# Kernel optimization log

Measured on AMD Instinct MI355X. Metric: run time of the kernel, lower is better.

## Reference

```python
import jax, jax.numpy as jnp
import numpy as np

D_MODEL = 2048
N_Q = 16
N_KV = 4
HEAD_DIM = 128
WINDOW = 512
ROPE_BASE = 10000.0


def _rope_cos_sin(T, dtype):
    half = HEAD_DIM // 2
    inv_freq = 1.0 / (ROPE_BASE ** (jnp.arange(0, half, dtype=jnp.float32) * 2.0 / HEAD_DIM))
    pos = jnp.arange(T, dtype=jnp.float32)
    ang = pos[:, None] * inv_freq[None, :]            # [T, half]
    emb = jnp.concatenate([ang, ang], axis=-1)        # [T, HEAD_DIM]
    return jnp.cos(emb).astype(dtype), jnp.sin(emb).astype(dtype)


def _rotate_half(x):
    x1, x2 = jnp.split(x, 2, axis=-1)
    return jnp.concatenate([-x2, x1], axis=-1)


def _apply_rope(t, cos, sin):
    # t: [B, H, T, hd]; cos/sin: [T, hd]
    return t * cos[None, None, :, :] + _rotate_half(t) * sin[None, None, :, :]


def setup_inputs() -> dict:
    key = jax.random.key(0)
    ks = jax.random.split(key, 5)
    s = 0.02
    return {
        "x": jax.random.normal(ks[0], (2, 2048, D_MODEL), dtype=jnp.float32),
        "wq": jax.random.normal(ks[1], (D_MODEL, N_Q * HEAD_DIM), dtype=jnp.float32) * s,
        "wk": jax.random.normal(ks[2], (D_MODEL, N_KV * HEAD_DIM), dtype=jnp.float32) * s,
        "wv": jax.random.normal(ks[3], (D_MODEL, N_KV * HEAD_DIM), dtype=jnp.float32) * s,
        "wo": jax.random.normal(ks[4], (N_Q * HEAD_DIM, D_MODEL), dtype=jnp.float32) * s,
    }


def reference(x, wq, wk, wv, wo):
    B, T, _ = x.shape
    q = (x @ wq).reshape(B, T, N_Q, HEAD_DIM).transpose(0, 2, 1, 3)    # [B,Hq,T,hd]
    k = (x @ wk).reshape(B, T, N_KV, HEAD_DIM).transpose(0, 2, 1, 3)   # [B,Hkv,T,hd]
    v = (x @ wv).reshape(B, T, N_KV, HEAD_DIM).transpose(0, 2, 1, 3)

    cos, sin = _rope_cos_sin(T, x.dtype)
    q = _apply_rope(q, cos, sin)
    k = _apply_rope(k, cos, sin)

    # GQA: repeat_interleave kv heads to match q heads
    g = N_Q // N_KV
    k = jnp.repeat(k, g, axis=1)
    v = jnp.repeat(v, g, axis=1)

    scale = 1.0 / np.sqrt(HEAD_DIM)
    scores = jnp.einsum("bhqd,bhkd->bhqk", q, k) * scale

    idx = jnp.arange(T)
    diff = idx[:, None] - idx[None, :]
    keep = (diff >= 0) & (diff < WINDOW)               # causal & sliding window
    scores = jnp.where(keep[None, None, :, :], scores, jnp.finfo(scores.dtype).min)
    attn = jax.nn.softmax(scores, axis=-1)

    out = jnp.einsum("bhqk,bhkd->bhqd", attn, v)       # [B,Hq,T,hd]
    out = out.transpose(0, 2, 1, 3).reshape(B, T, N_Q * HEAD_DIM)
    return out @ wo
```

## Files before the change

### kernel.cpp

```cpp
#include <hip/hip_runtime.h>

#define T_SEQ   2048
#define DM      2048
#define N_Q     16
#define N_KV    4
#define HD      128
#define WIN     512
#define NB      2
#define NQKV    3072
#define QK_SCALE_L2E 0.12751744f

typedef short bf16x8 __attribute__((ext_vector_type(8)));
typedef float f32x4  __attribute__((ext_vector_type(4)));
typedef float f32x16 __attribute__((ext_vector_type(16)));
typedef unsigned short us4v __attribute__((ext_vector_type(4)));

__device__ __forceinline__ unsigned short f2bf(float f) {
    union { float f; unsigned u; } v; v.f = f;
    unsigned u = v.u;
    u += 0x7fffu + ((u >> 16) & 1u);
    return (unsigned short)(u >> 16);
}
__device__ __forceinline__ float bf2f(unsigned short h) {
    union { unsigned u; float f; } v; v.u = ((unsigned)h) << 16;
    return v.f;
}
__device__ __forceinline__ unsigned cvt_pk_bf16(float a, float b) {
    unsigned r;
    asm("v_cvt_pk_bf16_f32 %0, %1, %2" : "=v"(r) : "v"(a), "v"(b));
    return r;
}

#define GLOAD_LDS16(g, l) __builtin_amdgcn_global_load_lds( \
    (const __attribute__((address_space(1))) void*)(g),     \
    (__attribute__((address_space(3))) void*)(l), 16, 0, 0)

struct us4 { unsigned short a, b, c, d; };


__global__ __launch_bounds__(256)
void prep_a(const float* __restrict__ x, const float* __restrict__ wq,
            const float* __restrict__ wk, const float* __restrict__ wv,
            const float* __restrict__ wo,
            unsigned short* __restrict__ xbf, unsigned short* __restrict__ wqkvT,
            unsigned short* __restrict__ woT,
            float* __restrict__ cosT, float* __restrict__ sinT) {
    __shared__ float tile[32][33];
    int blk = blockIdx.x;
    if (blk < 8192) {
        long i = ((long)blk * 256 + threadIdx.x) * 4;
        float4 f = *(const float4*)(x + i);
        us4 o; o.a = f2bf(f.x); o.b = f2bf(f.y); o.c = f2bf(f.z); o.d = f2bf(f.w);
        *(us4*)(xbf + i) = o;
        return;
    }
    blk -= 8192;
    if (blk < 10240) {
        const float* in; unsigned short* outp; int C, bx, by;
        if (blk < 4096)      { in = wq; outp = wqkvT;                         C = DM;  bx = blk & 63;          by = blk >> 6; }
        else if (blk < 5120) { int k = blk - 4096; in = wk; outp = wqkvT + (long)DM * DM;         C = 512; bx = k & 15; by = k >> 4; }
        else if (blk < 6144) { int k = blk - 5120; in = wv; outp = wqkvT + (long)(DM + 512) * DM; C = 512; bx = k & 15; by = k >> 4; }
        else                 { int k = blk - 6144; in = wo; outp = woT;                           C = DM;  bx = k & 63; by = k >> 6; }
        const int c0 = bx * 32, r0 = by * 32;
        const int tx = threadIdx.x & 31, ty = threadIdx.x >> 5;
#pragma unroll
        for (int i = 0; i < 4; ++i)
            tile[ty + i * 8][tx] = in[(long)(r0 + ty + i * 8) * C + c0 + tx];
        __syncthreads();
#pragma unroll
        for (int i = 0; i < 4; ++i)
            outp[(long)(c0 + ty + i * 8) * DM + r0 + tx] = f2bf(tile[tx][ty + i * 8]);
        return;
    }
    blk -= 10240;
    const int idx = blk * 256 + threadIdx.x;
    const int t = idx >> 6, d = idx & 63;
    const float inv = __expf(-(float)d * (9.210340371976184f / 64.0f));
    const float ang = (float)t * inv;
    cosT[idx] = cosf(ang);
    sinT[idx] = sinf(ang);
}


__global__ __launch_bounds__(256)
void prep_b(unsigned short* __restrict__ qkv,
            const float* __restrict__ cosT, const float* __restrict__ sinT,
            unsigned short* __restrict__ vt) {
    __shared__ unsigned short stile[32][33];
    int blk = blockIdx.x;
    if (blk < 5120) {
        const int idx = blk * 256 + threadIdx.x;
        const int d4 = (idx & 15) * 4;
        const int hh = (idx >> 4) % 20;
        const int row = idx / (16 * 20);
        const int t = row & (T_SEQ - 1);
        const int col = (hh < N_Q) ? hh * HD + d4 : DM + (hh - N_Q) * HD + d4;
        unsigned short* p = qkv + (long)row * NQKV + col;
        us4v a = *(const us4v*)p;
        us4v b = *(const us4v*)(p + 64);
        float4 c = *(const float4*)&cosT[t * 64 + d4];
        float4 s = *(const float4*)&sinT[t * 64 + d4];
        const float sc = (hh < N_Q) ? QK_SCALE_L2E : 1.0f;
        us4v o1, o2;
        const float cc[4] = { c.x, c.y, c.z, c.w }, ss[4] = { s.x, s.y, s.z, s.w };
#pragma unroll
        for (int i = 0; i < 4; ++i) {
            const float av = bf2f(a[i]), bv = bf2f(b[i]);
            o1[i] = f2bf((av * cc[i] - bv * ss[i]) * sc);
            o2[i] = f2bf((bv * cc[i] + av * ss[i]) * sc);
        }
        *(us4v*)p        = o1;
        *(us4v*)(p + 64) = o2;
        return;
    }
    blk -= 5120;
    const int bh = blk >> 8;
    const int d0 = ((blk >> 6) & 3) * 32;
    const int t0 = (blk & 63) * 32;
    const int tx = threadIdx.x & 31, ty = threadIdx.x >> 5;
    const long inbase = (long)(bh >> 2) * T_SEQ;
    const int coff = DM + N_KV * HD + (bh & 3) * HD;
#pragma unroll
    for (int i = 0; i < 4; ++i)
        stile[ty + i * 8][tx] = qkv[(inbase + t0 + ty + i * 8) * NQKV + coff + d0 + tx];
    __syncthreads();
#pragma unroll
    for (int i = 0; i < 4; ++i)
        vt[((long)bh * HD + d0 + ty + i * 8) * T_SEQ + t0 + tx] = stile[tx][ty + i * 8];
}


template<int OUT_BF16>
__global__ __launch_bounds__(256)
void gemm_bt(const unsigned short* __restrict__ A,
             const unsigned short* __restrict__ Bt,
             void* __restrict__ Cvoid, int K, int ldc) {
    __shared__ __align__(16) unsigned short sA[128 * 64];
    __shared__ __align__(16) unsigned short sB[128 * 64];
    const int tid = threadIdx.x;
    const int lane = tid & 63;
    const int wid = tid >> 6;
    const int wr = (wid >> 1) * 64, wc = (wid & 1) * 64;
    const int l5 = lane >> 5, l31 = lane & 31;

    const int gx = gridDim.x;
    const int nwg = gx * gridDim.y;
    int flat = blockIdx.y * gx + blockIdx.x;
    flat = (flat & 7) * (nwg >> 3) + (flat >> 3);
    const long Arow0 = (long)(flat / gx) * 128;
    const long Brow0 = (long)(flat % gx) * 128;

    f32x16 acc[2][2] = {};

    for (int kt = 0; kt < K; kt += 64) {
        __syncthreads();
#pragma unroll
        for (int n = 0; n < 4; ++n) {
            const int linb = n * 256 + wid * 64;
            const int lin  = linb + lane;
            const int row  = lin >> 3;
            const int sw   = (row ^ (row >> 3)) & 7;
            const int sc   = (lin & 7) ^ sw;
            const unsigned short* gA = A  + (Arow0 + row) * K + kt + sc * 8;
            const unsigned short* gB = Bt + (Brow0 + row) * K + kt + sc * 8;
            GLOAD_LDS16(gA, &sA[linb * 8]);
            GLOAD_LDS16(gB, &sB[linb * 8]);
        }
        __syncthreads();
#pragma unroll
        for (int kc = 0; kc < 4; ++kc) {
            bf16x8 av[2], bv[2];
#pragma unroll
            for (int t = 0; t < 2; ++t) {
                const int rowa = wr + t * 32 + l31;
                const int ca = (kc * 2 + l5) ^ ((rowa ^ (rowa >> 3)) & 7);
                av[t] = *(const bf16x8*)&sA[rowa * 64 + ca * 8];
                const int rowb = wc + t * 32 + l31;
                const int cb = (kc * 2 + l5) ^ ((rowb ^ (rowb >> 3)) & 7);
                bv[t] = *(const bf16x8*)&sB[rowb * 64 + cb * 8];
            }
#pragma unroll
            for (int ti = 0; ti < 2; ++ti)
#pragma unroll
                for (int tj = 0; tj < 2; ++tj)
                    acc[ti][tj] = __builtin_amdgcn_mfma_f32_32x32x16_bf16(av[ti], bv[tj], acc[ti][tj], 0, 0, 0);
        }
    }

#pragma unroll
    for (int ti = 0; ti < 2; ++ti)
#pragma unroll
        for (int tj = 0; tj < 2; ++tj)
#pragma unroll
            for (int r = 0; r < 16; ++r) {
                const long row = Arow0 + wr + ti * 32 + (r & 3) + 8 * (r >> 2) + 4 * l5;
                const long col = Brow0 + wc + tj * 32 + l31;
                if (OUT_BF16)
                    ((unsigned short*)Cvoid)[row * ldc + col] = f2bf(acc[ti][tj][r]);
                else
                    ((float*)Cvoid)[row * ldc + col] = acc[ti][tj][r];
            }
}


__global__ __launch_bounds__(512, 2)
void attn_kernel(const unsigned short* __restrict__ qkv,
                 const unsigned short* __restrict__ vt,
                 unsigned short* __restrict__ aout) {
    const int qt = blockIdx.x, hkv = blockIdx.y, b = blockIdx.z;
    const int tid = threadIdx.x, lane = tid & 63, w = tid >> 6;
    const int qh = hkv * 4 + (w & 3);
    const int qsub = w >> 2;
    const int q0w = qt * 64 + qsub * 32;
    const int lo = lane & 15, hi = lane >> 4;

    __shared__ __align__(16) unsigned short sK[2][64 * 128];
    __shared__ __align__(16) unsigned short sV[2][128 * 64];
    __shared__ __align__(16) unsigned short plds[8][32 * 64];
    unsigned short* pl = plds[w];

    bf16x8 qf2[2][4];
#pragma unroll
    for (int f = 0; f < 2; ++f) {
        const unsigned short* qp = qkv + (long)(b * T_SEQ + q0w + f * 16 + lo) * NQKV + qh * HD + hi * 8;
#pragma unroll
        for (int s = 0; s < 4; ++s) qf2[f][s] = *(const bf16x8*)(qp + s * 32);
    }

    f32x4 of[8][2] = {};
    float m_r[2] = { -1e30f, -1e30f };
    float s_r[2] = { 0.f, 0.f };

    int kstart = qt * 64 - (WIN - 1);
    if (kstart < 0) kstart = 0;
    kstart &= ~63;
    const int kend = qt * 64 + 63;

    const unsigned short* kbase = qkv + (long)b * T_SEQ * NQKV + DM + hkv * HD;
    const unsigned short* vbase = vt + (long)(b * N_KV + hkv) * HD * T_SEQ;

    int kr[2], kc[2], vr[2], vc[2];
#pragma unroll
    for (int u = 0; u < 2; ++u) {
        const int c = u * 512 + tid;
        kr[u] = c >> 4;  kc[u] = (c & 15) ^ (kr[u] & 7);
        vr[u] = c >> 3;  vc[u] = (c & 7) ^ (vr[u] & 7);
    }

#define STAGE(bf, kt_) do {                                                              \
    _Pragma("unroll")                                                                    \
    for (int u = 0; u < 2; ++u) {                                                        \
        const int dbase = (u * 512 + w * 64) * 8;                                        \
        GLOAD_LDS16(kbase + (long)((kt_) + kr[u]) * NQKV + kc[u] * 8, &sK[bf][dbase]);   \
        GLOAD_LDS16(vbase + (long)vr[u] * T_SEQ + (kt_) + vc[u] * 8, &sV[bf][dbase]);    \
    } } while (0)

    STAGE(0, kstart);
    asm volatile("s_waitcnt vmcnt(0)" ::: "memory");
    __syncthreads();

    int buf = 0;
    for (int kt = kstart; kt <= kend; kt += 64) {
        if (kt + 64 <= kend) STAGE(buf ^ 1, kt + 64);

        f32x4 sf[4][2] = {};
        __builtin_amdgcn_s_setprio(1);
#pragma unroll
        for (int n = 0; n < 4; ++n) {
            const int row = n * 16 + lo;
#pragma unroll
            for (int s = 0; s < 4; ++s) {
                const int c = (s * 4 + hi) ^ (row & 7);
                bf16x8 kf = *(const bf16x8*)&sK[buf][row * 128 + c * 8];
                sf[n][0] = __builtin_amdgcn_mfma_f32_16x16x32_bf16(kf, qf2[0][s], sf[n][0], 0, 0, 0);
                sf[n][1] = __builtin_amdgcn_mfma_f32_16x16x32_bf16(kf, qf2[1][s], sf[n][1], 0, 0, 0);
            }
        }
        __builtin_amdgcn_s_setprio(0);

        const bool nomask = ((kt + 63) <= q0w) && ((q0w + 31 - kt) < WIN);

        float pv[2][4][4];
        float mx[2] = { -1e30f, -1e30f };
        if (nomask) {
#pragma unroll
            for (int f = 0; f < 2; ++f)
#pragma unroll
                for (int n = 0; n < 4; ++n)
#pragma unroll
                    for (int r = 0; r < 4; ++r) {
                        pv[f][n][r] = sf[n][f][r];
                        mx[f] = fmaxf(mx[f], pv[f][n][r]);
                    }
        } else {
#pragma unroll
            for (int f = 0; f < 2; ++f) {
                const int q = q0w + f * 16 + lo;
#pragma unroll
                for (int n = 0; n < 4; ++n)
#pragma unroll
                    for (int r = 0; r < 4; ++r) {
                        const int d = q - (kt + n * 16 + hi * 4 + r);
                        pv[f][n][r] = (d >= 0 && d < WIN) ? sf[n][f][r] : -1e30f;
                        mx[f] = fmaxf(mx[f], pv[f][n][r]);
                    }
            }
        }
#pragma unroll
        for (int f = 0; f < 2; ++f) {
            mx[f] = fmaxf(mx[f], __shfl_xor(mx[f], 16));
            mx[f] = fmaxf(mx[f], __shfl_xor(mx[f], 32));
        }

        const bool ok = (mx[0] <= m_r[0] + 8.0f) && (mx[1] <= m_r[1] + 8.0f);
        if (!__all(ok)) {
#pragma unroll
            for (int f = 0; f < 2; ++f) {
                const float mnew = fmaxf(m_r[f], mx[f]);
                const float resc = exp2f(m_r[f] - mnew);
                s_r[f] *= resc;
                m_r[f] = mnew;
                float r4[4];
#pragma unroll
                for (int r = 0; r < 4; ++r) r4[r] = __shfl(resc, hi * 4 + r);
#pragma unroll
                for (int j = 0; j < 8; ++j) {
                    of[j][f][0] *= r4[0]; of[j][f][1] *= r4[1];
                    of[j][f][2] *= r4[2]; of[j][f][3] *= r4[3];
                }
            }
        }

#pragma unroll
        for (int f = 0; f < 2; ++f) {
            float psum = 0.f;
#pragma unroll
            for (int n = 0; n < 4; ++n)
#pragma unroll
                for (int r = 0; r < 4; ++r) {
                    pv[f][n][r] = exp2f(pv[f][n][r] - m_r[f]);
                    psum += pv[f][n][r];
                }
            psum += __shfl_xor(psum, 16);
            psum += __shfl_xor(psum, 32);
            s_r[f] += psum;
        }

        const int swz = (lo & 7) << 3;
#pragma unroll
        for (int f = 0; f < 2; ++f) {
            const int rowq = f * 16 + lo;
#pragma unroll
            for (int n = 0; n < 4; ++n) {
                const int k0 = n * 16 + hi * 4;
                *(unsigned*)&pl[rowq * 64 + (k0 ^ swz)]       = cvt_pk_bf16(pv[f][n][0], pv[f][n][1]);
                *(unsigned*)&pl[rowq * 64 + ((k0 + 2) ^ swz)] = cvt_pk_bf16(pv[f][n][2], pv[f][n][3]);
            }
        }
        asm volatile("s_waitcnt lgkmcnt(0)" ::: "memory");
        __builtin_amdgcn_sched_barrier(0);
        bf16x8 pa2[2][2];
#pragma unroll
        for (int f = 0; f < 2; ++f)
#pragma unroll
            for (int ks = 0; ks < 2; ++ks) {
                const int c = (ks * 4 + hi) ^ (lo & 7);
                pa2[f][ks] = *(const bf16x8*)&pl[(f * 16 + lo) * 64 + c * 8];
            }

        __builtin_amdgcn_s_setprio(1);
#pragma unroll
        for (int j = 0; j < 8; ++j) {
            const int row = j * 16 + lo;
#pragma unroll
            for (int ks = 0; ks < 2; ++ks) {
                const int c = (ks * 4 + hi) ^ (row & 7);
                bf16x8 vf = *(const bf16x8*)&sV[buf][row * 64 + c * 8];
                of[j][0] = __builtin_amdgcn_mfma_f32_16x16x32_bf16(pa2[0][ks], vf, of[j][0], 0, 0, 0);
                of[j][1] = __builtin_amdgcn_mfma_f32_16x16x32_bf16(pa2[1][ks], vf, of[j][1], 0, 0, 0);
            }
        }
        __builtin_amdgcn_s_setprio(0);

        asm volatile("s_waitcnt vmcnt(0)" ::: "memory");
        __syncthreads();
        buf ^= 1;
    }
#undef STAGE

#pragma unroll
    for (int f = 0; f < 2; ++f) {
        float s4[4];
#pragma unroll
        for (int r = 0; r < 4; ++r) s4[r] = __shfl(s_r[f], hi * 4 + r);
#pragma unroll
        for (int r = 0; r < 4; ++r) {
            const int qrow = q0w + f * 16 + hi * 4 + r;
            const float inv = 1.0f / s4[r];
            unsigned short* op = aout + (long)(b * T_SEQ + qrow) * DM + qh * HD + lo;
#pragma unroll
            for (int j = 0; j < 8; ++j) op[j * 16] = f2bf(of[j][f][r] * inv);
        }
    }
}


extern "C" void kernel_launch(void* const* d_in, const int* in_sizes, int n_in,
                              void* d_out, int out_size, void* d_ws, size_t ws_size,
                              hipStream_t stream) {
    (void)in_sizes; (void)n_in; (void)out_size; (void)ws_size;
    const float* x  = (const float*)d_in[0];
    const float* wq = (const float*)d_in[1];
    const float* wk = (const float*)d_in[2];
    const float* wv = (const float*)d_in[3];
    const float* wo = (const float*)d_in[4];
    float* out = (float*)d_out;
    char* ws = (char*)d_ws;

    unsigned short* xbf   = (unsigned short*)(ws);
    unsigned short* wqkvT = (unsigned short*)(ws + 16777216);
    unsigned short* woT   = (unsigned short*)(ws + 29360128);
    unsigned short* qkv   = (unsigned short*)(ws + 37748736);
    unsigned short* vt    = (unsigned short*)(ws + 62914560);
    unsigned short* aout  = (unsigned short*)(ws + 67108864);
    float* cosT = (float*)(ws + 83886080);
    float* sinT = (float*)(ws + 84410368);

    prep_a<<<dim3(18944), dim3(256), 0, stream>>>(x, wq, wk, wv, wo, xbf, wqkvT, woT, cosT, sinT);
    gemm_bt<1><<<dim3(NQKV / 128, 32), dim3(256), 0, stream>>>(xbf, wqkvT, qkv, DM, NQKV);
    prep_b<<<dim3(7168), dim3(256), 0, stream>>>(qkv, cosT, sinT, vt);
    attn_kernel<<<dim3(T_SEQ / 64, 4, 2), dim3(512), 0, stream>>>(qkv, vt, aout);
    gemm_bt<0><<<dim3(DM / 128, 32), dim3(256), 0, stream>>>(aout, woT, out, DM, DM);
}
```

Baseline: 162.8 us.

## Fuse RoPE and Q scaling into the QKV GEMM epilogue

The QKV projection GEMM becomes a specialized kernel whose warps own columns d and d+64 of each head, so the RoPE rotation and the Q scale are applied to the fp32 accumulators before the bf16 store. The prep_b kernel shrinks to only the V transpose. This removes a full read-modify-write pass over Q and K and one double bf16 rounding, in exchange for strided B-operand fragment reads and cos/sin loads in the GEMM epilogue.

```diff
diff --git a/kernel.cpp b/kernel.cpp
--- a/kernel.cpp
+++ b/kernel.cpp
@@ -83,37 +83,9 @@
 
 
 __global__ __launch_bounds__(256)
-void prep_b(unsigned short* __restrict__ qkv,
-            const float* __restrict__ cosT, const float* __restrict__ sinT,
-            unsigned short* __restrict__ vt) {
+void prep_b(const unsigned short* __restrict__ qkv, unsigned short* __restrict__ vt) {
     __shared__ unsigned short stile[32][33];
-    int blk = blockIdx.x;
-    if (blk < 5120) {
-        const int idx = blk * 256 + threadIdx.x;
-        const int d4 = (idx & 15) * 4;
-        const int hh = (idx >> 4) % 20;
-        const int row = idx / (16 * 20);
-        const int t = row & (T_SEQ - 1);
-        const int col = (hh < N_Q) ? hh * HD + d4 : DM + (hh - N_Q) * HD + d4;
-        unsigned short* p = qkv + (long)row * NQKV + col;
-        us4v a = *(const us4v*)p;
-        us4v b = *(const us4v*)(p + 64);
-        float4 c = *(const float4*)&cosT[t * 64 + d4];
-        float4 s = *(const float4*)&sinT[t * 64 + d4];
-        const float sc = (hh < N_Q) ? QK_SCALE_L2E : 1.0f;
-        us4v o1, o2;
-        const float cc[4] = { c.x, c.y, c.z, c.w }, ss[4] = { s.x, s.y, s.z, s.w };
-#pragma unroll
-        for (int i = 0; i < 4; ++i) {
-            const float av = bf2f(a[i]), bv = bf2f(b[i]);
-            o1[i] = f2bf((av * cc[i] - bv * ss[i]) * sc);
-            o2[i] = f2bf((bv * cc[i] + av * ss[i]) * sc);
-        }
-        *(us4v*)p        = o1;
-        *(us4v*)(p + 64) = o2;
-        return;
-    }
-    blk -= 5120;
+    const int blk = blockIdx.x;
     const int bh = blk >> 8;
     const int d0 = ((blk >> 6) & 3) * 32;
     const int t0 = (blk & 63) * 32;
@@ -130,17 +102,19 @@
 }
 
 
-template<int OUT_BF16>
 __global__ __launch_bounds__(256)
-void gemm_bt(const unsigned short* __restrict__ A,
-             const unsigned short* __restrict__ Bt,
-             void* __restrict__ Cvoid, int K, int ldc) {
+void gemm_qkv(const unsigned short* __restrict__ A,
+              const unsigned short* __restrict__ Bt,
+              unsigned short* __restrict__ C,
+              const float* __restrict__ cosT, const float* __restrict__ sinT) {
+    const int K = DM, ldc = NQKV;
     __shared__ __align__(16) unsigned short sA[128 * 64];
     __shared__ __align__(16) unsigned short sB[128 * 64];
     const int tid = threadIdx.x;
     const int lane = tid & 63;
     const int wid = tid >> 6;
-    const int wr = (wid >> 1) * 64, wc = (wid & 1) * 64;
+    const int wr  = (wid >> 1) * 64;
+    const int wcs = (wid & 1) * 32;
     const int l5 = lane >> 5, l31 = lane & 31;
 
     const int gx = gridDim.x;
@@ -175,6 +149,94 @@
                 const int rowa = wr + t * 32 + l31;
                 const int ca = (kc * 2 + l5) ^ ((rowa ^ (rowa >> 3)) & 7);
                 av[t] = *(const bf16x8*)&sA[rowa * 64 + ca * 8];
+                const int rowb = wcs + t * 64 + l31;
+                const int cb = (kc * 2 + l5) ^ ((rowb ^ (rowb >> 3)) & 7);
+                bv[t] = *(const bf16x8*)&sB[rowb * 64 + cb * 8];
+            }
+#pragma unroll
+            for (int ti = 0; ti < 2; ++ti)
+#pragma unroll
+                for (int tj = 0; tj < 2; ++tj)
+                    acc[ti][tj] = __builtin_amdgcn_mfma_f32_32x32x16_bf16(av[ti], bv[tj], acc[ti][tj], 0, 0, 0);
+        }
+    }
+
+    const int hb = (int)(Brow0 >> 7);
+    if (hb < 20) {
+        const float sc = (hb < 16) ? QK_SCALE_L2E : 1.0f;
+        const int d6 = wcs + l31;
+        const long colL = Brow0 + d6;
+#pragma unroll
+        for (int ti = 0; ti < 2; ++ti)
+#pragma unroll
+            for (int r = 0; r < 16; ++r) {
+                const long row = Arow0 + wr + ti * 32 + (r & 3) + 8 * (r >> 2) + 4 * l5;
+                const int t = (int)(row & (T_SEQ - 1));
+                const float c = cosT[t * 64 + d6];
+                const float s = sinT[t * 64 + d6];
+                const float a = acc[ti][0][r], b = acc[ti][1][r];
+                C[row * ldc + colL]      = f2bf((a * c - b * s) * sc);
+                C[row * ldc + colL + 64] = f2bf((b * c + a * s) * sc);
+            }
+    } else {
+#pragma unroll
+        for (int ti = 0; ti < 2; ++ti)
+#pragma unroll
+            for (int tj = 0; tj < 2; ++tj)
+#pragma unroll
+                for (int r = 0; r < 16; ++r) {
+                    const long row = Arow0 + wr + ti * 32 + (r & 3) + 8 * (r >> 2) + 4 * l5;
+                    const long col = Brow0 + wcs + tj * 64 + l31;
+                    C[row * ldc + col] = f2bf(acc[ti][tj][r]);
+                }
+    }
+}
+
+
+__global__ __launch_bounds__(256)
+void gemm_bt(const unsigned short* __restrict__ A,
+             const unsigned short* __restrict__ Bt,
+             float* __restrict__ C, int K, int ldc) {
+    __shared__ __align__(16) unsigned short sA[128 * 64];
+    __shared__ __align__(16) unsigned short sB[128 * 64];
+    const int tid = threadIdx.x;
+    const int lane = tid & 63;
+    const int wid = tid >> 6;
+    const int wr = (wid >> 1) * 64, wc = (wid & 1) * 64;
+    const int l5 = lane >> 5, l31 = lane & 31;
+
+    const int gx = gridDim.x;
+    const int nwg = gx * gridDim.y;
+    int flat = blockIdx.y * gx + blockIdx.x;
+    flat = (flat & 7) * (nwg >> 3) + (flat >> 3);
+    const long Arow0 = (long)(flat / gx) * 128;
+    const long Brow0 = (long)(flat % gx) * 128;
+
+    f32x16 acc[2][2] = {};
+
+    for (int kt = 0; kt < K; kt += 64) {
+        __syncthreads();
+#pragma unroll
+        for (int n = 0; n < 4; ++n) {
+            const int linb = n * 256 + wid * 64;
+            const int lin  = linb + lane;
+            const int row  = lin >> 3;
+            const int sw   = (row ^ (row >> 3)) & 7;
+            const int sc   = (lin & 7) ^ sw;
+            const unsigned short* gA = A  + (Arow0 + row) * K + kt + sc * 8;
+            const unsigned short* gB = Bt + (Brow0 + row) * K + kt + sc * 8;
+            GLOAD_LDS16(gA, &sA[linb * 8]);
+            GLOAD_LDS16(gB, &sB[linb * 8]);
+        }
+        __syncthreads();
+#pragma unroll
+        for (int kc = 0; kc < 4; ++kc) {
+            bf16x8 av[2], bv[2];
+#pragma unroll
+            for (int t = 0; t < 2; ++t) {
+                const int rowa = wr + t * 32 + l31;
+                const int ca = (kc * 2 + l5) ^ ((rowa ^ (rowa >> 3)) & 7);
+                av[t] = *(const bf16x8*)&sA[rowa * 64 + ca * 8];
                 const int rowb = wc + t * 32 + l31;
                 const int cb = (kc * 2 + l5) ^ ((rowb ^ (rowb >> 3)) & 7);
                 bv[t] = *(const bf16x8*)&sB[rowb * 64 + cb * 8];
@@ -195,10 +257,7 @@
             for (int r = 0; r < 16; ++r) {
                 const long row = Arow0 + wr + ti * 32 + (r & 3) + 8 * (r >> 2) + 4 * l5;
                 const long col = Brow0 + wc + tj * 32 + l31;
-                if (OUT_BF16)
-                    ((unsigned short*)Cvoid)[row * ldc + col] = f2bf(acc[ti][tj][r]);
-                else
-                    ((float*)Cvoid)[row * ldc + col] = acc[ti][tj][r];
+                C[row * ldc + col] = acc[ti][tj][r];
             }
 }
 
@@ -427,8 +486,8 @@
     float* sinT = (float*)(ws + 84410368);
 
     prep_a<<<dim3(18944), dim3(256), 0, stream>>>(x, wq, wk, wv, wo, xbf, wqkvT, woT, cosT, sinT);
-    gemm_bt<1><<<dim3(NQKV / 128, 32), dim3(256), 0, stream>>>(xbf, wqkvT, qkv, DM, NQKV);
-    prep_b<<<dim3(7168), dim3(256), 0, stream>>>(qkv, cosT, sinT, vt);
+    gemm_qkv<<<dim3(NQKV / 128, 32), dim3(256), 0, stream>>>(xbf, wqkvT, qkv, cosT, sinT);
+    prep_b<<<dim3(2048), dim3(256), 0, stream>>>(qkv, vt);
     attn_kernel<<<dim3(T_SEQ / 64, 4, 2), dim3(512), 0, stream>>>(qkv, vt, aout);
-    gemm_bt<0><<<dim3(DM / 128, 32), dim3(256), 0, stream>>>(aout, woT, out, DM, DM);
-}
+    gemm_bt<<<dim3(DM / 128, 32), dim3(256), 0, stream>>>(aout, woT, out, DM, DM);
+}
```

Result: slower. 175.8 us (+8.0%).
